# Kernel tuning notes

Measured on AMD Instinct MI355X. Metric: run time of the kernel, lower is better.

The kernel has to match this reference:

```python
import jax, jax.numpy as jnp
import numpy as np

B, S = 16, 4096
E_ENC, E_DEC, H = 1024, 1024, 512


def setup_inputs() -> dict:
    key = jax.random.key(0)
    ks = jax.random.split(key, 8)
    sc_e = 1.0 / np.sqrt(E_ENC)
    sc_d = 1.0 / np.sqrt(E_DEC)
    sc_h = 1.0 / np.sqrt(H)
    return {
        "encoder_hiddens": jax.random.normal(ks[0], (B, S, E_ENC), jnp.float32),
        "decoder_hidden": jax.random.normal(ks[1], (B, E_DEC), jnp.float32),
        "We": jax.random.uniform(ks[2], (E_ENC, H), jnp.float32, -sc_e, sc_e),
        "be": jax.random.uniform(ks[3], (H,), jnp.float32, -sc_e, sc_e),
        "Wd": jax.random.uniform(ks[4], (E_DEC, H), jnp.float32, -sc_d, sc_d),
        "bd": jax.random.uniform(ks[5], (H,), jnp.float32, -sc_d, sc_d),
        "Wo": jax.random.uniform(ks[6], (H, 1), jnp.float32, -sc_h, sc_h),
        "bo": jax.random.uniform(ks[7], (1,), jnp.float32, -sc_h, sc_h),
    }


def reference(encoder_hiddens, decoder_hidden, We, be, Wd, bd, Wo, bo):
    # Additive (Bahdanau) attention.
    # enc_proj: [B,S,H]; dec_proj: [B,1,H] broadcast over sequence.
    enc_proj = jnp.einsum("bse,eh->bsh", encoder_hiddens, We) + be
    dec_proj = jnp.einsum("bd,dh->bh", decoder_hidden, Wd) + bd
    e = jnp.tanh(enc_proj + dec_proj[:, None, :])          # [B,S,H]
    scores = jnp.einsum("bsh,h->bs", e, Wo[:, 0]) + bo[0]  # [B,S]
    attn = jax.nn.softmax(scores, axis=-1)                 # [B,S]
    context = jnp.einsum("bs,bse->be", attn, encoder_hiddens)  # [B,E_ENC]
    return context
```

## Files before the change

### kernel.cpp

```cpp
#include <hip/hip_runtime.h>
#include <hip/hip_bf16.h>
#include <math.h>

#define B_ 16
#define S_ 4096
#define E_ 1024
#define H_ 512

#define BM 256
#define BN 256
#define BK 64
#define NCHUNK (E_ / BK)

typedef short bf16x8 __attribute__((ext_vector_type(8)));
typedef unsigned short u16x8 __attribute__((ext_vector_type(8)));
typedef float f32x4 __attribute__((ext_vector_type(4)));

__device__ inline unsigned short f2bf(float x) {
    __hip_bfloat16 h = __float2bfloat16(x);
    return *(unsigned short*)&h;
}
__device__ inline float bf2f(unsigned short u) {
    unsigned int x = ((unsigned int)u) << 16;
    float f;
    __builtin_memcpy(&f, &x, 4);
    return f;
}

#define GLD16(g, l_) __builtin_amdgcn_global_load_lds(                     \
    (const __attribute__((address_space(1))) void*)(g),                    \
    (__attribute__((address_space(3))) void*)(l_), 16, 0, 0)

#define BAR() do { asm volatile("" ::: "memory");                          \
                   __builtin_amdgcn_s_barrier();                           \
                   asm volatile("" ::: "memory"); } while (0)

__global__ __launch_bounds__(256) void prep_conv_kernel(
    const float* __restrict__ enc, const float* __restrict__ We,
    const float* __restrict__ dec, const float* __restrict__ Wd,
    const float* __restrict__ bd, const float* __restrict__ be,
    unsigned short* __restrict__ WeTcB, float* __restrict__ dp,
    unsigned short* __restrict__ encB) {
    __shared__ float red[4][64];
    int bid = blockIdx.x, t = threadIdx.x;
    if (bid < 64) {
        int c = bid >> 2, n0t = (bid & 3) * 128;
#pragma unroll 4
        for (int it = 0; it < 32; ++it) {
            int o = it * 256 + t;
            int n_rel = o >> 6, within = o & 63;
            int cp = within >> 3, j = within & 7;
            int n = n0t + n_rel;
            int k = c * 64 + ((cp ^ (n & 7)) << 3) + j;
            WeTcB[c * 32768 + n * 64 + within] = f2bf(We[(size_t)k * H_ + n]);
        }
    } else if (bid < 192) {
        int id = bid - 64;
        int b = id >> 3, hc = id & 7;
        int h = hc * 64 + (t & 63);
        int ec = t >> 6;
        const float* dr = dec + b * E_ + ec * 256;
        const float* wp = Wd + (size_t)(ec * 256) * H_ + h;
        float acc = 0.f;
#pragma unroll 8
        for (int e = 0; e < 256; ++e) acc = fmaf(dr[e], wp[(size_t)e * H_], acc);
        red[ec][t & 63] = acc;
        __syncthreads();
        if (t < 64) {
            int hh = hc * 64 + t;
            dp[b * H_ + hh] = red[0][t] + red[1][t] + red[2][t] + red[3][t] + bd[hh] + be[hh];
        }
    } else {
        size_t base = ((size_t)(bid - 192) * 256 + t) * 16;
        const float* ep = enc + base;
        unsigned short* op = encB + base;
        float4 v0 = *(const float4*)(ep);
        float4 v1 = *(const float4*)(ep + 4);
        float4 v2 = *(const float4*)(ep + 8);
        float4 v3 = *(const float4*)(ep + 12);
        u16x8 u0, u1;
        u0[0] = f2bf(v0.x); u0[1] = f2bf(v0.y); u0[2] = f2bf(v0.z); u0[3] = f2bf(v0.w);
        u0[4] = f2bf(v1.x); u0[5] = f2bf(v1.y); u0[6] = f2bf(v1.z); u0[7] = f2bf(v1.w);
        u1[0] = f2bf(v2.x); u1[1] = f2bf(v2.y); u1[2] = f2bf(v2.z); u1[3] = f2bf(v2.w);
        u1[4] = f2bf(v3.x); u1[5] = f2bf(v3.y); u1[6] = f2bf(v3.z); u1[7] = f2bf(v3.w);
        *(u16x8*)(op) = u0;
        *(u16x8*)(op + 8) = u1;
    }
}

__global__ __launch_bounds__(512, 2) void scores_gemm_kernel(
    const unsigned short* __restrict__ encB, const unsigned short* __restrict__ WeTcB,
    const float* __restrict__ Wo, const float* __restrict__ dp,
    float* __restrict__ parts) {
    __shared__ unsigned short sA[2][BM * BK];
    __shared__ unsigned short sB[2][BN * BK];
    __shared__ float sRed[4][BM];

    int tid = threadIdx.x;
    int w8 = tid >> 6, l = tid & 63;
    int l16 = l & 15, quad = l >> 4;
    int wm = w8 >> 2, wn = w8 & 3;
    int lrow = l >> 3, lcp = l & 7;

    int bid = blockIdx.x;
    int xcd = bid & 7;
    int sq = bid >> 3;
    int nt = sq & 1;
    int mt = ((sq >> 1) << 3) + xcd;
    size_t m0 = (size_t)mt * BM;
    int n0 = nt * BN;
    int b = mt >> 4;

    const unsigned short* gA_base = encB + (m0 + (size_t)(w8 * 8 + lrow)) * E_ + (lcp ^ lrow) * 8;
    const unsigned short* gB_base = WeTcB + (size_t)(n0 + w8 * 8) * BK + l * 8;

#define STAGE_A(bb, tt, hh) do {                                               \
        const unsigned short* _s = gA_base + (size_t)((hh) * 128) * E_ + (tt) * BK; \
        GLD16(_s, &sA[bb][((hh) * 128 + w8 * 8) * BK]);                        \
        GLD16(_s + (size_t)64 * E_, &sA[bb][((hh) * 128 + 64 + w8 * 8) * BK]); \
    } while (0)
#define STAGE_B(bb, tt, hh) do {                                               \
        const unsigned short* _s = gB_base + (size_t)(tt) * (H_ * BK) + (hh) * 128 * BK; \
        GLD16(_s, &sB[bb][((hh) * 128 + w8 * 8) * BK]);                        \
        GLD16(_s + 64 * BK, &sB[bb][((hh) * 128 + 64 + w8 * 8) * BK]);         \
    } while (0)

    f32x4 acc[8][4];
#pragma unroll
    for (int i = 0; i < 8; ++i)
#pragma unroll
        for (int j = 0; j < 4; ++j) acc[i][j] = (f32x4)0.f;

    int aOff = (wm * 128 + l16) * BK;
    int bOff = (wn * 64 + l16) * BK;
    int sw = l16 & 7;
    int kq0 = ((quad ^ sw) << 3);
    int kq1 = (((4 + quad) ^ sw) << 3);

    STAGE_A(0, 0, 0); STAGE_A(0, 0, 1); STAGE_B(0, 0, 0); STAGE_B(0, 0, 1);
    STAGE_B(1, 1, 0); STAGE_A(1, 1, 0); STAGE_A(1, 1, 1);
    asm volatile("s_waitcnt vmcnt(6)" ::: "memory");
    BAR();

    for (int t = 0; t < NCHUNK; ++t) {
        int cur = t & 1, nxt = cur ^ 1;
        const unsigned short* sAc = sA[cur];
        const unsigned short* sBc = sB[cur];
        bf16x8 aF[4][2], bF[4][2];

#pragma unroll
        for (int im = 0; im < 4; ++im) {
            aF[im][0] = *(const bf16x8*)(sAc + aOff + im * 1024 + kq0);
            aF[im][1] = *(const bf16x8*)(sAc + aOff + im * 1024 + kq1);
        }
#pragma unroll
        for (int jn = 0; jn < 2; ++jn) {
            bF[jn][0] = *(const bf16x8*)(sBc + bOff + jn * 1024 + kq0);
            bF[jn][1] = *(const bf16x8*)(sBc + bOff + jn * 1024 + kq1);
        }
        if (t + 1 < NCHUNK) STAGE_B(nxt, t + 1, 1);
        BAR();
        __builtin_amdgcn_s_setprio(1);
#pragma unroll
        for (int ks = 0; ks < 2; ++ks)
#pragma unroll
            for (int im = 0; im < 4; ++im)
#pragma unroll
                for (int jn = 0; jn < 2; ++jn)
                    acc[im][jn] = __builtin_amdgcn_mfma_f32_16x16x32_bf16(
                        aF[im][ks], bF[jn][ks], acc[im][jn], 0, 0, 0);
        __builtin_amdgcn_s_setprio(0);
        BAR();

#pragma unroll
        for (int jn = 0; jn < 2; ++jn) {
            bF[2 + jn][0] = *(const bf16x8*)(sBc + bOff + (2 + jn) * 1024 + kq0);
            bF[2 + jn][1] = *(const bf16x8*)(sBc + bOff + (2 + jn) * 1024 + kq1);
        }
        BAR();
        __builtin_amdgcn_s_setprio(1);
#pragma unroll
        for (int ks = 0; ks < 2; ++ks)
#pragma unroll
            for (int im = 0; im < 4; ++im)
#pragma unroll
                for (int jn = 0; jn < 2; ++jn)
                    acc[im][2 + jn] = __builtin_amdgcn_mfma_f32_16x16x32_bf16(
                        aF[im][ks], bF[2 + jn][ks], acc[im][2 + jn], 0, 0, 0);
        __builtin_amdgcn_s_setprio(0);
        BAR();

#pragma unroll
        for (int im = 0; im < 4; ++im) {
            aF[im][0] = *(const bf16x8*)(sAc + aOff + (4 + im) * 1024 + kq0);
            aF[im][1] = *(const bf16x8*)(sAc + aOff + (4 + im) * 1024 + kq1);
        }
        if (t + 2 < NCHUNK) STAGE_B(cur, t + 2, 0);
        BAR();
        __builtin_amdgcn_s_setprio(1);
#pragma unroll
        for (int ks = 0; ks < 2; ++ks)
#pragma unroll
            for (int im = 0; im < 4; ++im)
#pragma unroll
                for (int jn = 0; jn < 2; ++jn)
                    acc[4 + im][jn] = __builtin_amdgcn_mfma_f32_16x16x32_bf16(
                        aF[im][ks], bF[jn][ks], acc[4 + im][jn], 0, 0, 0);
        __builtin_amdgcn_s_setprio(0);
        BAR();

        if (t + 2 < NCHUNK) { STAGE_A(cur, t + 2, 0); STAGE_A(cur, t + 2, 1); }
        __builtin_amdgcn_s_setprio(1);
#pragma unroll
        for (int ks = 0; ks < 2; ++ks)
#pragma unroll
            for (int im = 0; im < 4; ++im)
#pragma unroll
                for (int jn = 0; jn < 2; ++jn)
                    acc[4 + im][2 + jn] = __builtin_amdgcn_mfma_f32_16x16x32_bf16(
                        aF[im][ks], bF[2 + jn][ks], acc[4 + im][2 + jn], 0, 0, 0);
        __builtin_amdgcn_s_setprio(0);
        if (t < NCHUNK - 2) {
            asm volatile("s_waitcnt vmcnt(6)" ::: "memory");
        } else if (t == NCHUNK - 2) {
            asm volatile("s_waitcnt vmcnt(0)" ::: "memory");
        }
        if (t < NCHUNK - 1) BAR();
    }
#undef STAGE_A
#undef STAGE_B

    float dpv[4], wov[4];
    const float* dpb = dp + b * H_;
#pragma unroll
    for (int jn = 0; jn < 4; ++jn) {
        int h = n0 + wn * 64 + jn * 16 + l16;
        dpv[jn] = dpb[h];
        wov[jn] = Wo[h];
    }
#pragma unroll
    for (int im = 0; im < 8; ++im)
#pragma unroll
        for (int r = 0; r < 4; ++r) {
            float s = 0.f;
#pragma unroll
            for (int jn = 0; jn < 4; ++jn) {
                float x = acc[im][jn][r] + dpv[jn];
                float e = __expf(2.f * x);
                s += (1.f - 2.f / (e + 1.f)) * wov[jn];
            }
            s += __shfl_xor(s, 1, 64);
            s += __shfl_xor(s, 2, 64);
            s += __shfl_xor(s, 4, 64);
            s += __shfl_xor(s, 8, 64);
            if (l16 == 0) sRed[wn][wm * 128 + im * 16 + quad * 4 + r] = s;
        }
    __syncthreads();
    if (tid < BM) {
        int s_in = (int)(m0 & (S_ - 1)) + tid;
        parts[(size_t)(nt * B_ + b) * S_ + s_in] =
            sRed[0][tid] + sRed[1][tid] + sRed[2][tid] + sRed[3][tid];
    }
}

__global__ __launch_bounds__(256) void stats_kernel(const float* __restrict__ parts,
                                                    float2* __restrict__ stats) {
    int b = blockIdx.x, tid = threadIdx.x;
    const float4* p0 = (const float4*)(parts + (size_t)(0 * B_ + b) * S_);
    const float4* p1 = (const float4*)(parts + (size_t)(1 * B_ + b) * S_);
    float4 v[4];
    float m = -1e30f;
#pragma unroll
    for (int i = 0; i < 4; ++i) {
        int idx = i * 256 + tid;
        float4 a0 = p0[idx], a1 = p1[idx];
        v[i].x = a0.x + a1.x;
        v[i].y = a0.y + a1.y;
        v[i].z = a0.z + a1.z;
        v[i].w = a0.w + a1.w;
        m = fmaxf(m, fmaxf(fmaxf(v[i].x, v[i].y), fmaxf(v[i].z, v[i].w)));
    }
    for (int off = 32; off; off >>= 1) m = fmaxf(m, __shfl_xor(m, off, 64));
    __shared__ float redm[4];
    __shared__ float reds[4];
    if ((tid & 63) == 0) redm[tid >> 6] = m;
    __syncthreads();
    m = fmaxf(fmaxf(redm[0], redm[1]), fmaxf(redm[2], redm[3]));
    float s = 0.f;
#pragma unroll
    for (int i = 0; i < 4; ++i) {
        s += __expf(v[i].x - m) + __expf(v[i].y - m);
        s += __expf(v[i].z - m) + __expf(v[i].w - m);
    }
    for (int off = 32; off; off >>= 1) s += __shfl_xor(s, off, 64);
    if ((tid & 63) == 0) reds[tid >> 6] = s;
    __syncthreads();
    if (tid == 0) {
        stats[b] = make_float2(m, reds[0] + reds[1] + reds[2] + reds[3]);
    }
}

__global__ __launch_bounds__(256) void ctx_partial_bf16(
    const unsigned short* __restrict__ encB, const float* __restrict__ parts,
    const float2* __restrict__ stats, float* __restrict__ part) {
    int b = blockIdx.x >> 5;
    int c = blockIdx.x & 31;
    int s0 = c * 128;
    int tid = threadIdx.x;
    __shared__ float w[128];
    if (tid < 128) {
        size_t idx = (size_t)b * S_ + s0 + tid;
        float x = parts[idx] + parts[(size_t)B_ * S_ + idx];
        w[tid] = __expf(x - stats[b].x);
    }
    __syncthreads();
    int e8 = (tid & 127) * 8;
    int sh = tid >> 7;
    const unsigned short* base = encB + ((size_t)b * S_ + s0 + sh * 64) * E_ + e8;
    const float* wp = w + sh * 64;
    float acc[8];
#pragma unroll
    for (int t = 0; t < 8; ++t) acc[t] = 0.f;
    for (int s = 0; s < 64; s += 8) {
        u16x8 v[8];
#pragma unroll
        for (int u = 0; u < 8; ++u) v[u] = *(const u16x8*)(base + (size_t)(s + u) * E_);
#pragma unroll
        for (int u = 0; u < 8; ++u) {
            float ws = wp[s + u];
#pragma unroll
            for (int t = 0; t < 8; ++t) acc[t] = fmaf(ws, bf2f(v[u][t]), acc[t]);
        }
    }
    float* po = part + ((size_t)(b * 64 + c * 2 + sh)) * E_ + e8;
    *(float4*)(po) = make_float4(acc[0], acc[1], acc[2], acc[3]);
    *(float4*)(po + 4) = make_float4(acc[4], acc[5], acc[6], acc[7]);
}

__global__ __launch_bounds__(256) void ctx_reduce(const float* __restrict__ part,
                                                  const float2* __restrict__ stats,
                                                  float* __restrict__ out) {
    int idx = blockIdx.x * 256 + threadIdx.x;
    int b = idx >> 10;
    int e = idx & 1023;
    const float* p = part + (size_t)b * 64 * E_ + e;
    float s0 = 0.f, s1 = 0.f, s2 = 0.f, s3 = 0.f;
    for (int c = 0; c < 64; c += 4) {
        s0 += p[(size_t)(c + 0) * E_];
        s1 += p[(size_t)(c + 1) * E_];
        s2 += p[(size_t)(c + 2) * E_];
        s3 += p[(size_t)(c + 3) * E_];
    }
    out[idx] = ((s0 + s1) + (s2 + s3)) * (1.f / stats[b].y);
}

extern "C" void kernel_launch(void* const* d_in, const int* in_sizes, int n_in,
                              void* d_out, int out_size, void* d_ws, size_t ws_size,
                              hipStream_t stream) {
    const float* enc = (const float*)d_in[0];
    const float* dec = (const float*)d_in[1];
    const float* We  = (const float*)d_in[2];
    const float* be  = (const float*)d_in[3];
    const float* Wd  = (const float*)d_in[4];
    const float* bd  = (const float*)d_in[5];
    const float* Wo  = (const float*)d_in[6];
    float* out = (float*)d_out;

    char* wsp = (char*)d_ws;
    unsigned short* WeTcB = (unsigned short*)wsp;
    float* dp = (float*)(wsp + (1 << 20));
    float2* stats = (float2*)(wsp + (1 << 20) + (32 << 10));
    float* parts = (float*)(wsp + (1 << 20) + (64 << 10));
    float* part = (float*)(wsp + (4 << 20));
    unsigned short* encB = (unsigned short*)(wsp + (8 << 20));

    prep_conv_kernel<<<192 + 16384, 256, 0, stream>>>(enc, We, dec, Wd, bd, be,
                                                      WeTcB, dp, encB);
    scores_gemm_kernel<<<(B_ * S_ / BM) * (H_ / BN), 512, 0, stream>>>(
        encB, WeTcB, Wo, dp, parts);
    stats_kernel<<<B_, 256, 0, stream>>>(parts, stats);
    ctx_partial_bf16<<<B_ * 32, 256, 0, stream>>>(encB, parts, stats, part);
    ctx_reduce<<<B_ * E_ / 256, 256, 0, stream>>>(part, stats, out);
}
```

Measured before the change: 489.2 us.

## Fuse fp32-to-bf16 encoder conversion into GEMM A-tile staging

Drops the separate pass that converted the whole encoder tensor to bf16. The scores GEMM now loads fp32 encoder tiles into registers, converts them to bf16 and writes them to LDS with the same swizzle, prefetching the next chunk during the current compute. The context kernel reads fp32 encoder data directly. This removes one write and one read of the bf16 copy, but the GEMM reads twice the bytes for A, loses the direct global-to-LDS path, uses more registers, and the context pass reads fp32.

```diff
diff --git a/kernel.cpp b/kernel.cpp
--- a/kernel.cpp
+++ b/kernel.cpp
@@ -20,12 +20,6 @@
     __hip_bfloat16 h = __float2bfloat16(x);
     return *(unsigned short*)&h;
 }
-__device__ inline float bf2f(unsigned short u) {
-    unsigned int x = ((unsigned int)u) << 16;
-    float f;
-    __builtin_memcpy(&f, &x, 4);
-    return f;
-}
 
 #define GLD16(g, l_) __builtin_amdgcn_global_load_lds(                     \
     (const __attribute__((address_space(1))) void*)(g),                    \
@@ -35,12 +29,11 @@
                    __builtin_amdgcn_s_barrier();                           \
                    asm volatile("" ::: "memory"); } while (0)
 
-__global__ __launch_bounds__(256) void prep_conv_kernel(
-    const float* __restrict__ enc, const float* __restrict__ We,
-    const float* __restrict__ dec, const float* __restrict__ Wd,
-    const float* __restrict__ bd, const float* __restrict__ be,
-    unsigned short* __restrict__ WeTcB, float* __restrict__ dp,
-    unsigned short* __restrict__ encB) {
+__global__ __launch_bounds__(256) void prep_kernel(
+    const float* __restrict__ We, const float* __restrict__ dec,
+    const float* __restrict__ Wd, const float* __restrict__ bd,
+    const float* __restrict__ be, unsigned short* __restrict__ WeTcB,
+    float* __restrict__ dp) {
     __shared__ float red[4][64];
     int bid = blockIdx.x, t = threadIdx.x;
     if (bid < 64) {
@@ -54,7 +47,7 @@
             int k = c * 64 + ((cp ^ (n & 7)) << 3) + j;
             WeTcB[c * 32768 + n * 64 + within] = f2bf(We[(size_t)k * H_ + n]);
         }
-    } else if (bid < 192) {
+    } else {
         int id = bid - 64;
         int b = id >> 3, hc = id & 7;
         int h = hc * 64 + (t & 63);
@@ -70,26 +63,11 @@
             int hh = hc * 64 + t;
             dp[b * H_ + hh] = red[0][t] + red[1][t] + red[2][t] + red[3][t] + bd[hh] + be[hh];
         }
-    } else {
-        size_t base = ((size_t)(bid - 192) * 256 + t) * 16;
-        const float* ep = enc + base;
-        unsigned short* op = encB + base;
-        float4 v0 = *(const float4*)(ep);
-        float4 v1 = *(const float4*)(ep + 4);
-        float4 v2 = *(const float4*)(ep + 8);
-        float4 v3 = *(const float4*)(ep + 12);
-        u16x8 u0, u1;
-        u0[0] = f2bf(v0.x); u0[1] = f2bf(v0.y); u0[2] = f2bf(v0.z); u0[3] = f2bf(v0.w);
-        u0[4] = f2bf(v1.x); u0[5] = f2bf(v1.y); u0[6] = f2bf(v1.z); u0[7] = f2bf(v1.w);
-        u1[0] = f2bf(v2.x); u1[1] = f2bf(v2.y); u1[2] = f2bf(v2.z); u1[3] = f2bf(v2.w);
-        u1[4] = f2bf(v3.x); u1[5] = f2bf(v3.y); u1[6] = f2bf(v3.z); u1[7] = f2bf(v3.w);
-        *(u16x8*)(op) = u0;
-        *(u16x8*)(op + 8) = u1;
     }
 }
 
 __global__ __launch_bounds__(512, 2) void scores_gemm_kernel(
-    const unsigned short* __restrict__ encB, const unsigned short* __restrict__ WeTcB,
+    const float* __restrict__ enc, const unsigned short* __restrict__ WeTcB,
     const float* __restrict__ Wo, const float* __restrict__ dp,
     float* __restrict__ parts) {
     __shared__ unsigned short sA[2][BM * BK];
@@ -111,19 +89,34 @@
     int n0 = nt * BN;
     int b = mt >> 4;
 
-    const unsigned short* gA_base = encB + (m0 + (size_t)(w8 * 8 + lrow)) * E_ + (lcp ^ lrow) * 8;
+    const float* gA = enc + (m0 + (size_t)(w8 * 8 + lrow)) * E_ + lcp * 8;
     const unsigned short* gB_base = WeTcB + (size_t)(n0 + w8 * 8) * BK + l * 8;
-
-#define STAGE_A(bb, tt, hh) do {                                               \
-        const unsigned short* _s = gA_base + (size_t)((hh) * 128) * E_ + (tt) * BK; \
-        GLD16(_s, &sA[bb][((hh) * 128 + w8 * 8) * BK]);                        \
-        GLD16(_s + (size_t)64 * E_, &sA[bb][((hh) * 128 + 64 + w8 * 8) * BK]); \
-    } while (0)
+    int awOff = (w8 * 8 + lrow) * BK + ((lcp ^ lrow) << 3);
+
 #define STAGE_B(bb, tt, hh) do {                                               \
         const unsigned short* _s = gB_base + (size_t)(tt) * (H_ * BK) + (hh) * 128 * BK; \
         GLD16(_s, &sB[bb][((hh) * 128 + w8 * 8) * BK]);                        \
         GLD16(_s + 64 * BK, &sB[bb][((hh) * 128 + 64 + w8 * 8) * BK]);         \
     } while (0)
+#define ISSUE_A(tt) do {                                                       \
+        const float* _p = gA + (tt) * BK;                                      \
+        _Pragma("unroll")                                                      \
+        for (int g = 0; g < 4; ++g) {                                          \
+            av[2 * g]     = *(const float4*)(_p + (size_t)(g * 64) * E_);      \
+            av[2 * g + 1] = *(const float4*)(_p + (size_t)(g * 64) * E_ + 4);  \
+        }                                                                      \
+    } while (0)
+#define WRITE_A(bb) do {                                                       \
+        _Pragma("unroll")                                                      \
+        for (int g = 0; g < 4; ++g) {                                          \
+            u16x8 _u;                                                          \
+            _u[0] = f2bf(av[2 * g].x);     _u[1] = f2bf(av[2 * g].y);          \
+            _u[2] = f2bf(av[2 * g].z);     _u[3] = f2bf(av[2 * g].w);          \
+            _u[4] = f2bf(av[2 * g + 1].x); _u[5] = f2bf(av[2 * g + 1].y);      \
+            _u[6] = f2bf(av[2 * g + 1].z); _u[7] = f2bf(av[2 * g + 1].w);      \
+            *(u16x8*)(&sA[bb][awOff + g * 64 * BK]) = _u;                      \
+        }                                                                      \
+    } while (0)
 
     f32x4 acc[8][4];
 #pragma unroll
@@ -137,10 +130,12 @@
     int kq0 = ((quad ^ sw) << 3);
     int kq1 = (((4 + quad) ^ sw) << 3);
 
-    STAGE_A(0, 0, 0); STAGE_A(0, 0, 1); STAGE_B(0, 0, 0); STAGE_B(0, 0, 1);
-    STAGE_B(1, 1, 0); STAGE_A(1, 1, 0); STAGE_A(1, 1, 1);
-    asm volatile("s_waitcnt vmcnt(6)" ::: "memory");
-    BAR();
+    float4 av[8];
+    STAGE_B(0, 0, 0); STAGE_B(0, 0, 1);
+    ISSUE_A(0);
+    WRITE_A(0);
+    asm volatile("s_waitcnt vmcnt(0) lgkmcnt(0)" ::: "memory");
+    __builtin_amdgcn_s_barrier();
 
     for (int t = 0; t < NCHUNK; ++t) {
         int cur = t & 1, nxt = cur ^ 1;
@@ -148,6 +143,10 @@
         const unsigned short* sBc = sB[cur];
         bf16x8 aF[4][2], bF[4][2];
 
+        if (t + 1 < NCHUNK) {
+            STAGE_B(nxt, t + 1, 0); STAGE_B(nxt, t + 1, 1);
+            ISSUE_A(t + 1);
+        }
 #pragma unroll
         for (int im = 0; im < 4; ++im) {
             aF[im][0] = *(const bf16x8*)(sAc + aOff + im * 1024 + kq0);
@@ -158,7 +157,6 @@
             bF[jn][0] = *(const bf16x8*)(sBc + bOff + jn * 1024 + kq0);
             bF[jn][1] = *(const bf16x8*)(sBc + bOff + jn * 1024 + kq1);
         }
-        if (t + 1 < NCHUNK) STAGE_B(nxt, t + 1, 1);
         BAR();
         __builtin_amdgcn_s_setprio(1);
 #pragma unroll
@@ -195,7 +193,6 @@
             aF[im][0] = *(const bf16x8*)(sAc + aOff + (4 + im) * 1024 + kq0);
             aF[im][1] = *(const bf16x8*)(sAc + aOff + (4 + im) * 1024 + kq1);
         }
-        if (t + 2 < NCHUNK) STAGE_B(cur, t + 2, 0);
         BAR();
         __builtin_amdgcn_s_setprio(1);
 #pragma unroll
@@ -209,7 +206,7 @@
         __builtin_amdgcn_s_setprio(0);
         BAR();
 
-        if (t + 2 < NCHUNK) { STAGE_A(cur, t + 2, 0); STAGE_A(cur, t + 2, 1); }
+        if (t + 1 < NCHUNK) WRITE_A(nxt);
         __builtin_amdgcn_s_setprio(1);
 #pragma unroll
         for (int ks = 0; ks < 2; ++ks)
@@ -220,15 +217,14 @@
                     acc[4 + im][2 + jn] = __builtin_amdgcn_mfma_f32_16x16x32_bf16(
                         aF[im][ks], bF[2 + jn][ks], acc[4 + im][2 + jn], 0, 0, 0);
         __builtin_amdgcn_s_setprio(0);
-        if (t < NCHUNK - 2) {
-            asm volatile("s_waitcnt vmcnt(6)" ::: "memory");
-        } else if (t == NCHUNK - 2) {
-            asm volatile("s_waitcnt vmcnt(0)" ::: "memory");
-        }
-        if (t < NCHUNK - 1) BAR();
-    }
-#undef STAGE_A
+        if (t + 1 < NCHUNK) {
+            asm volatile("s_waitcnt lgkmcnt(0)" ::: "memory");
+            __builtin_amdgcn_s_barrier();
+        }
+    }
 #undef STAGE_B
+#undef ISSUE_A
+#undef WRITE_A
 
     float dpv[4], wov[4];
     const float* dpb = dp + b * H_;
@@ -300,8 +296,8 @@
     }
 }
 
-__global__ __launch_bounds__(256) void ctx_partial_bf16(
-    const unsigned short* __restrict__ encB, const float* __restrict__ parts,
+__global__ __launch_bounds__(256) void ctx_partial_f32(
+    const float* __restrict__ enc, const float* __restrict__ parts,
     const float2* __restrict__ stats, float* __restrict__ part) {
     int b = blockIdx.x >> 5;
     int c = blockIdx.x & 31;
@@ -316,20 +312,29 @@
     __syncthreads();
     int e8 = (tid & 127) * 8;
     int sh = tid >> 7;
-    const unsigned short* base = encB + ((size_t)b * S_ + s0 + sh * 64) * E_ + e8;
+    const float* base = enc + ((size_t)b * S_ + s0 + sh * 64) * E_ + e8;
     const float* wp = w + sh * 64;
     float acc[8];
 #pragma unroll
     for (int t = 0; t < 8; ++t) acc[t] = 0.f;
-    for (int s = 0; s < 64; s += 8) {
-        u16x8 v[8];
-#pragma unroll
-        for (int u = 0; u < 8; ++u) v[u] = *(const u16x8*)(base + (size_t)(s + u) * E_);
-#pragma unroll
-        for (int u = 0; u < 8; ++u) {
+    for (int s = 0; s < 64; s += 4) {
+        float4 v0[4], v1[4];
+#pragma unroll
+        for (int u = 0; u < 4; ++u) {
+            v0[u] = *(const float4*)(base + (size_t)(s + u) * E_);
+            v1[u] = *(const float4*)(base + (size_t)(s + u) * E_ + 4);
+        }
+#pragma unroll
+        for (int u = 0; u < 4; ++u) {
             float ws = wp[s + u];
-#pragma unroll
-            for (int t = 0; t < 8; ++t) acc[t] = fmaf(ws, bf2f(v[u][t]), acc[t]);
+            acc[0] = fmaf(ws, v0[u].x, acc[0]);
+            acc[1] = fmaf(ws, v0[u].y, acc[1]);
+            acc[2] = fmaf(ws, v0[u].z, acc[2]);
+            acc[3] = fmaf(ws, v0[u].w, acc[3]);
+            acc[4] = fmaf(ws, v1[u].x, acc[4]);
+            acc[5] = fmaf(ws, v1[u].y, acc[5]);
+            acc[6] = fmaf(ws, v1[u].z, acc[6]);
+            acc[7] = fmaf(ws, v1[u].w, acc[7]);
         }
     }
     float* po = part + ((size_t)(b * 64 + c * 2 + sh)) * E_ + e8;
@@ -372,13 +377,11 @@
     float2* stats = (float2*)(wsp + (1 << 20) + (32 << 10));
     float* parts = (float*)(wsp + (1 << 20) + (64 << 10));
     float* part = (float*)(wsp + (4 << 20));
-    unsigned short* encB = (unsigned short*)(wsp + (8 << 20));
-
-    prep_conv_kernel<<<192 + 16384, 256, 0, stream>>>(enc, We, dec, Wd, bd, be,
-                                                      WeTcB, dp, encB);
+
+    prep_kernel<<<192, 256, 0, stream>>>(We, dec, Wd, bd, be, WeTcB, dp);
     scores_gemm_kernel<<<(B_ * S_ / BM) * (H_ / BN), 512, 0, stream>>>(
-        encB, WeTcB, Wo, dp, parts);
+        enc, WeTcB, Wo, dp, parts);
     stats_kernel<<<B_, 256, 0, stream>>>(parts, stats);
-    ctx_partial_bf16<<<B_ * 32, 256, 0, stream>>>(encB, parts, stats, part);
+    ctx_partial_f32<<<B_ * 32, 256, 0, stream>>>(enc, parts, stats, part);
     ctx_reduce<<<B_ * E_ / 256, 256, 0, stream>>>(part, stats, out);
 }
```

Measured after the change: 507.6 us. +3.8%, slower.
